# Optimization experiments

Hardware: AMD Instinct MI355X
Metric: run time of the kernel (lower is better)

## Reference

```python
import jax, jax.numpy as jnp
import numpy as np

N_NODES = 100000
ORDER = 2


def _spmm(edge_src, edge_dst, edge_weight, x):
    # out[dst] += w * x[src]  ==  adj @ x  with adj in COO form
    msgs = edge_weight[:, None] * x[edge_src]          # [E, d]
    return jax.ops.segment_sum(msgs, edge_dst, num_segments=N_NODES)


def setup_inputs() -> dict:
    key = jax.random.key(0)
    k1, k2, k3, k4 = jax.random.split(key, 4)
    x = jax.random.normal(k1, (N_NODES, 32), dtype=jnp.float32)
    edge_src = jax.random.randint(k2, (1600000,), 0, N_NODES, dtype=jnp.int32)
    edge_dst = jax.random.randint(k3, (1600000,), 0, N_NODES, dtype=jnp.int32)
    edge_weight = jax.random.uniform(k4, (1600000,), dtype=jnp.float32)
    return {"x": x, "edge_src": edge_src, "edge_dst": edge_dst,
            "edge_weight": edge_weight}


def reference(x, edge_src, edge_dst, edge_weight):
    # SGConvolution.forward: x = spmm(adj, x) repeated `order` times
    for _ in range(ORDER):
        x = _spmm(edge_src, edge_dst, edge_weight, x)
    return x
```

## Files before the change

### kernel.cpp

```cpp
#include <hip/hip_runtime.h>

#define N_NODES 100000
#define NEDGE   1600000
#define D       32

#define BSHIFT   7
#define BNODES   128
#define NBUCKET  ((N_NODES + BNODES - 1) / BNODES)
#define NB_PAD   784
#define EPB      8192
#define CBLK     ((NEDGE + EPB - 1) / EPB)
#define CAP      3072

__global__ void bucket_hist_kernel(const int* __restrict__ dst, int* __restrict__ bucket_cnt) {
    __shared__ int h[NB_PAD];
    for (int i = threadIdx.x; i < NB_PAD; i += blockDim.x) h[i] = 0;
    __syncthreads();
    for (int e = blockIdx.x * blockDim.x + threadIdx.x; e < NEDGE; e += gridDim.x * blockDim.x)
        atomicAdd(&h[dst[e] >> BSHIFT], 1);
    __syncthreads();
    for (int i = threadIdx.x; i < NB_PAD; i += blockDim.x)
        if (h[i]) atomicAdd(&bucket_cnt[i], h[i]);
}

__global__ void bucket_scan_kernel(const int* __restrict__ bucket_cnt,
                                   int* __restrict__ bucket_off, int* __restrict__ bucket_cur) {
    __shared__ int s[1024];
    int tid = threadIdx.x;
    int v = (tid < NB_PAD) ? bucket_cnt[tid] : 0;
    s[tid] = v;
    __syncthreads();
    for (int o = 1; o < 1024; o <<= 1) {
        int t = (tid >= o) ? s[tid - o] : 0;
        __syncthreads();
        s[tid] += t;
        __syncthreads();
    }
    if (tid < NB_PAD) {
        int excl = s[tid] - v;
        bucket_off[tid] = excl;
        bucket_cur[tid] = excl;
    }
}

__global__ void bin_edges_kernel(const int* __restrict__ src, const int* __restrict__ dst,
                                 const float* __restrict__ w,
                                 int* __restrict__ bucket_cur, int2* __restrict__ binned) {
    __shared__ int cnt[NB_PAD];
    __shared__ int base[NB_PAD];
    int tid = threadIdx.x;
    for (int i = tid; i < NB_PAD; i += blockDim.x) cnt[i] = 0;
    __syncthreads();
    int e0 = blockIdx.x * EPB;
    for (int i = tid; i < EPB; i += blockDim.x) {
        int e = e0 + i;
        if (e < NEDGE) atomicAdd(&cnt[dst[e] >> BSHIFT], 1);
    }
    __syncthreads();
    for (int i = tid; i < NB_PAD; i += blockDim.x) {
        int c = cnt[i];
        base[i] = c ? atomicAdd(&bucket_cur[i], c) : 0;
        cnt[i] = 0;
    }
    __syncthreads();
    for (int i = tid; i < EPB; i += blockDim.x) {
        int e = e0 + i;
        if (e < NEDGE) {
            int d = dst[e];
            int b = d >> BSHIFT;
            int r = atomicAdd(&cnt[b], 1);
            binned[base[b] + r] = make_int2(src[e] | ((d & (BNODES - 1)) << 17),
                                            __float_as_int(w[e]));
        }
    }
}

__global__ void build_csr_kernel(const int* __restrict__ bucket_off, const int* __restrict__ bucket_cnt,
                                 const int2* __restrict__ binned,
                                 int2* __restrict__ csr, int* __restrict__ off, int* __restrict__ deg) {
    __shared__ int2 stage[CAP];
    __shared__ int2 sorted[CAP];
    __shared__ int ndcnt[BNODES];
    __shared__ int ndoff[BNODES];
    __shared__ int s[BNODES];

    int b = blockIdx.x;
    int tid = threadIdx.x;
    int start = bucket_off[b];
    int cnt_b = bucket_cnt[b];
    bool fast = (cnt_b <= CAP);

    if (tid < BNODES) ndcnt[tid] = 0;
    if (fast)
        for (int i = tid; i < cnt_b; i += blockDim.x) stage[i] = binned[start + i];
    __syncthreads();

    if (fast) {
        for (int i = tid; i < cnt_b; i += blockDim.x)
            atomicAdd(&ndcnt[(stage[i].x >> 17) & (BNODES - 1)], 1);
    } else {
        for (int i = tid; i < cnt_b; i += blockDim.x)
            atomicAdd(&ndcnt[(binned[start + i].x >> 17) & (BNODES - 1)], 1);
    }
    __syncthreads();

    int v = (tid < BNODES) ? ndcnt[tid] : 0;
    if (tid < BNODES) s[tid] = v;
    __syncthreads();
    for (int o = 1; o < BNODES; o <<= 1) {
        int t = (tid < BNODES && tid >= o) ? s[tid - o] : 0;
        __syncthreads();
        if (tid < BNODES) s[tid] += t;
        __syncthreads();
    }
    if (tid < BNODES) {
        ndoff[tid] = s[tid] - v;
        int node = b * BNODES + tid;
        if (node < N_NODES) {
            off[node] = start + ndoff[tid];
            deg[node] = v;
        }
        ndcnt[tid] = 0;
    }
    __syncthreads();

    if (fast) {
        for (int i = tid; i < cnt_b; i += blockDim.x) {
            int2 p = stage[i];
            int dl = (p.x >> 17) & (BNODES - 1);
            int r = atomicAdd(&ndcnt[dl], 1);
            sorted[ndoff[dl] + r] = make_int2(p.x & 0x1FFFF, p.y);
        }
        __syncthreads();
        for (int i = tid; i < cnt_b; i += blockDim.x) csr[start + i] = sorted[i];
    } else {
        for (int i = tid; i < cnt_b; i += blockDim.x) {
            int2 p = binned[start + i];
            int dl = (p.x >> 17) & (BNODES - 1);
            int r = atomicAdd(&ndcnt[dl], 1);
            csr[start + ndoff[dl] + r] = make_int2(p.x & 0x1FFFF, p.y);
        }
    }
}

__global__ void spmm_gather_kernel(const int* __restrict__ off, const int* __restrict__ deg,
                                   const int2* __restrict__ csr_sw,
                                   const float* __restrict__ x, float* __restrict__ out) {
    int gid = blockIdx.x * blockDim.x + threadIdx.x;
    if (gid >= N_NODES * 8) return;
    int node = gid >> 3;
    int c    = gid & 7;
    int start = off[node];
    int len   = deg[node];
    float4 acc = {0.f, 0.f, 0.f, 0.f};
    int k = 0;
    for (; k + 2 <= len; k += 2) {
        int2 sw0 = csr_sw[start + k];
        int2 sw1 = csr_sw[start + k + 1];
        const float4 xv0 = *reinterpret_cast<const float4*>(&x[(long)sw0.x * D + c * 4]);
        const float4 xv1 = *reinterpret_cast<const float4*>(&x[(long)sw1.x * D + c * 4]);
        float w0 = __int_as_float(sw0.y);
        float w1 = __int_as_float(sw1.y);
        acc.x += w0 * xv0.x; acc.y += w0 * xv0.y; acc.z += w0 * xv0.z; acc.w += w0 * xv0.w;
        acc.x += w1 * xv1.x; acc.y += w1 * xv1.y; acc.z += w1 * xv1.z; acc.w += w1 * xv1.w;
    }
    if (k < len) {
        int2 sw = csr_sw[start + k];
        const float4 xv = *reinterpret_cast<const float4*>(&x[(long)sw.x * D + c * 4]);
        float wt = __int_as_float(sw.y);
        acc.x += wt * xv.x; acc.y += wt * xv.y; acc.z += wt * xv.z; acc.w += wt * xv.w;
    }
    *reinterpret_cast<float4*>(&out[(long)node * D + c * 4]) = acc;
}

__global__ void spmm_scatter_kernel(const int* __restrict__ src, const int* __restrict__ dst,
                                    const float* __restrict__ w, const float* __restrict__ x,
                                    float* __restrict__ out) {
    long gid = (long)blockIdx.x * blockDim.x + threadIdx.x;
    if (gid >= (long)NEDGE * 8) return;
    int e = (int)(gid >> 3);
    int c = (int)(gid & 7);
    int s = src[e], d = dst[e];
    float wt = w[e];
    const float4 xv = *reinterpret_cast<const float4*>(&x[(long)s * D + c * 4]);
    float* o = &out[(long)d * D + c * 4];
    atomicAdd(o + 0, wt * xv.x);
    atomicAdd(o + 1, wt * xv.y);
    atomicAdd(o + 2, wt * xv.z);
    atomicAdd(o + 3, wt * xv.w);
}

extern "C" void kernel_launch(void* const* d_in, const int* in_sizes, int n_in,
                              void* d_out, int out_size, void* d_ws, size_t ws_size,
                              hipStream_t stream) {
    const float* x    = (const float*)d_in[0];
    const int*   esrc = (const int*)d_in[1];
    const int*   edst = (const int*)d_in[2];
    const float* ew   = (const float*)d_in[3];
    float* out = (float*)d_out;

    char* ws = (char*)d_ws;
    const size_t y_bytes = (size_t)N_NODES * D * sizeof(float);
    const size_t n_ints  = (size_t)N_NODES * sizeof(int);
    const size_t b_ints  = (size_t)NB_PAD * sizeof(int);
    const size_t e_sw    = (size_t)NEDGE * sizeof(int2);

    size_t o = 0;
    float* y          = (float*)(ws + o); o += y_bytes;
    int2*  csr        = (int2*) (ws + o); o += e_sw;
    int*   off        = (int*)  (ws + o); o += n_ints;
    int*   deg        = (int*)  (ws + o); o += n_ints;
    int*   bucket_cnt = (int*)  (ws + o); o += b_ints;
    int*   bucket_off = (int*)  (ws + o); o += b_ints;
    int*   bucket_cur = (int*)  (ws + o); o += b_ints;
    int2*  binned     = (int2*)y;

    if (ws_size < o) {
        hipMemsetAsync(y, 0, y_bytes, stream);
        hipMemsetAsync(out, 0, y_bytes, stream);
        const long total = (long)NEDGE * 8;
        const int blocks = (int)((total + 255) / 256);
        spmm_scatter_kernel<<<blocks, 256, 0, stream>>>(esrc, edst, ew, x, y);
        spmm_scatter_kernel<<<blocks, 256, 0, stream>>>(esrc, edst, ew, y, out);
        return;
    }

    hipMemsetAsync(bucket_cnt, 0, b_ints, stream);

    bucket_hist_kernel<<<256, 256, 0, stream>>>(edst, bucket_cnt);
    bucket_scan_kernel<<<1, 1024, 0, stream>>>(bucket_cnt, bucket_off, bucket_cur);
    bin_edges_kernel<<<CBLK, 256, 0, stream>>>(esrc, edst, ew, bucket_cur, binned);
    build_csr_kernel<<<NBUCKET, 256, 0, stream>>>(bucket_off, bucket_cnt, binned, csr, off, deg);

    const int gblocks = (N_NODES * 8 + 255) / 256;
    spmm_gather_kernel<<<gblocks, 256, 0, stream>>>(off, deg, csr, x, y);
    spmm_gather_kernel<<<gblocks, 256, 0, stream>>>(off, deg, csr, y, out);
}
```

Measured before the change: 138.9 us.

## Stage binned edges in shared memory for coalesced global scatter writes

The binning kernel now counting-sorts each block's edges into shared memory first and then writes them out contiguously. Each output run per bucket becomes consecutive, so writes to global memory are mostly coalesced instead of scattered. The dst values are also kept in registers so dst is read only once. The cost is about 82KB of LDS per block, which lowers occupancy, plus an in-block scan and extra barriers.

```diff
diff --git a/kernel.cpp b/kernel.cpp
--- a/kernel.cpp
+++ b/kernel.cpp
@@ -9,6 +9,7 @@
 #define NBUCKET  ((N_NODES + BNODES - 1) / BNODES)
 #define NB_PAD   784
 #define EPB      8192
+#define EPT      (EPB / 256)
 #define CBLK     ((NEDGE + EPB - 1) / EPB)
 #define CAP      3072
 
@@ -43,35 +44,81 @@
     }
 }
 
-__global__ void bin_edges_kernel(const int* __restrict__ src, const int* __restrict__ dst,
-                                 const float* __restrict__ w,
-                                 int* __restrict__ bucket_cur, int2* __restrict__ binned) {
+__global__ __launch_bounds__(256) void bin_edges_kernel(
+        const int* __restrict__ src, const int* __restrict__ dst,
+        const float* __restrict__ w,
+        int* __restrict__ bucket_cur, int2* __restrict__ binned) {
+    __shared__ int2 sorted[EPB];
+    __shared__ unsigned short bucketOf[EPB];
     __shared__ int cnt[NB_PAD];
-    __shared__ int base[NB_PAD];
-    int tid = threadIdx.x;
-    for (int i = tid; i < NB_PAD; i += blockDim.x) cnt[i] = 0;
-    __syncthreads();
-    int e0 = blockIdx.x * EPB;
-    for (int i = tid; i < EPB; i += blockDim.x) {
-        int e = e0 + i;
-        if (e < NEDGE) atomicAdd(&cnt[dst[e] >> BSHIFT], 1);
-    }
-    __syncthreads();
-    for (int i = tid; i < NB_PAD; i += blockDim.x) {
-        int c = cnt[i];
-        base[i] = c ? atomicAdd(&bucket_cur[i], c) : 0;
-        cnt[i] = 0;
-    }
-    __syncthreads();
-    for (int i = tid; i < EPB; i += blockDim.x) {
-        int e = e0 + i;
-        if (e < NEDGE) {
-            int d = dst[e];
+    __shared__ int ndoff[NB_PAD];
+    __shared__ int delta[NB_PAD];
+    __shared__ int partial[256];
+
+    const int tid = threadIdx.x;
+    const int e0  = blockIdx.x * EPB;
+    const int total = min(EPB, NEDGE - e0);
+
+    for (int i = tid; i < NB_PAD; i += 256) cnt[i] = 0;
+    __syncthreads();
+
+    int myd[EPT];
+    #pragma unroll
+    for (int it = 0; it < EPT; ++it) {
+        int e = e0 + it * 256 + tid;
+        myd[it] = (e < NEDGE) ? dst[e] : -1;
+        if (myd[it] >= 0) atomicAdd(&cnt[myd[it] >> BSHIFT], 1);
+    }
+    __syncthreads();
+
+    {
+        int b0 = tid * 4;
+        int c0 = 0, c1 = 0, c2 = 0, c3 = 0, s = 0;
+        if (b0 < NB_PAD) { c0 = cnt[b0]; c1 = cnt[b0+1]; c2 = cnt[b0+2]; c3 = cnt[b0+3];
+                           s = c0 + c1 + c2 + c3; }
+        partial[tid] = s;
+        __syncthreads();
+        int v = s;
+        for (int o = 1; o < 256; o <<= 1) {
+            int t2 = (tid >= o) ? partial[tid - o] : 0;
+            __syncthreads();
+            partial[tid] += t2;
+            __syncthreads();
+        }
+        int run = partial[tid] - v;
+        if (b0 < NB_PAD) {
+            int cs[4] = {c0, c1, c2, c3};
+            #pragma unroll
+            for (int j = 0; j < 4; ++j) {
+                int b = b0 + j;
+                ndoff[b] = run;
+                if (cs[j] > 0) delta[b] = atomicAdd(&bucket_cur[b], cs[j]) - run;
+                cnt[b] = 0;
+                run += cs[j];
+            }
+        }
+    }
+    __syncthreads();
+
+    #pragma unroll
+    for (int it = 0; it < EPT; ++it) {
+        int d = myd[it];
+        if (d >= 0) {
+            int e = e0 + it * 256 + tid;
             int b = d >> BSHIFT;
             int r = atomicAdd(&cnt[b], 1);
-            binned[base[b] + r] = make_int2(src[e] | ((d & (BNODES - 1)) << 17),
-                                            __float_as_int(w[e]));
-        }
+            int loc = ndoff[b] + r;
+            sorted[loc]   = make_int2(src[e] | ((d & (BNODES - 1)) << 17),
+                                      __float_as_int(w[e]));
+            bucketOf[loc] = (unsigned short)b;
+        }
+    }
+    __syncthreads();
+
+    for (int i = tid; i < total; i += 256) {
+        int2 v = sorted[i];
+        int  b = bucketOf[i];
+        binned[delta[b] + i] = v;
     }
 }
 
```

Result: slower. 142.3 us (+2.5%).
